# Kernel tuning notes

Hardware: AMD Instinct MI355X
Metric: run time of the kernel (lower is better)

The kernel has to match this reference:

```python
import jax, jax.numpy as jnp
import numpy as np
import math

NEG = -10000.0  # original uses -10000.0, not -inf

def setup_inputs() -> dict:
    key = jax.random.key(0)
    B, S, H, D = 2, 2048, 16, 128
    qkv = jax.random.normal(key, (B, S, 3, H, D), dtype=jnp.float32)
    return {"qkv": qkv}

def reference(qkv):
    # qkv: (B, S, 3, H, D); causal softmax attention, dropout p=0 (identity)
    B, S, _, H, D = qkv.shape
    q = qkv[:, :, 0]  # (B,S,H,D)
    k = qkv[:, :, 1]
    v = qkv[:, :, 2]
    softmax_scale = 1.0 / math.sqrt(D)
    # scores: (B, H, T, S)
    scores = jnp.einsum('bthd,bshd->bhts', q, k * softmax_scale)
    causal_mask = jnp.triu(jnp.full((S, S), NEG, dtype=scores.dtype), 1)
    scores = scores + causal_mask  # broadcast over (B,H)
    attention = jax.nn.softmax(scores, axis=-1)
    out = jnp.einsum('bhts,bshd->bthd', attention, v)  # (B,T,H,D)
    return out
```

## Files before the change

kernel.cpp:

```cpp
#include <hip/hip_runtime.h>
#include <hip/hip_bf16.h>
#include <math.h>

typedef __bf16 bf16;
typedef bf16 bf16x8 __attribute__((ext_vector_type(8)));
typedef float floatx4 __attribute__((ext_vector_type(4)));

#define MFMA16(a, b, c) __builtin_amdgcn_mfma_f32_16x16x32_bf16(a, b, c, 0, 0, 0)

constexpr int Bb = 2, Ss = 2048, Hh = 16, Dd = 128;
constexpr float SCALE = 0.08838834764831845f;

__global__ __launch_bounds__(256) void prep_pack(const float* __restrict__ qkv,
                                                 bf16* __restrict__ QP,
                                                 bf16* __restrict__ KP,
                                                 bf16* __restrict__ VP) {
  const int tid = threadIdx.x;
  const int w = tid >> 6, lane = tid & 63, quad = lane >> 4, l15 = lane & 15;
  const int qt = blockIdx.x, bh = blockIdx.y;
  const int b = bh >> 4, h = bh & 15;
  const int q0 = qt * 64;
  const size_t rs = (size_t)3 * Hh * Dd;
  const float* base = qkv + (size_t)b * Ss * rs + (size_t)h * Dd;

  {
    bf16* blob = QP + (size_t)(bh * 32 + qt) * 8192;
    const float* src = base + (size_t)(q0 + 4 * l15 + w) * rs;
    for (int kk = 0; kk < 4; ++kk) {
      const float* s8 = src + kk * 32 + quad * 8;
      float4 x0 = *(const float4*)s8, x1 = *(const float4*)(s8 + 4);
      bf16x8 f;
      f[0] = (bf16)(x0.x * SCALE); f[1] = (bf16)(x0.y * SCALE);
      f[2] = (bf16)(x0.z * SCALE); f[3] = (bf16)(x0.w * SCALE);
      f[4] = (bf16)(x1.x * SCALE); f[5] = (bf16)(x1.y * SCALE);
      f[6] = (bf16)(x1.z * SCALE); f[7] = (bf16)(x1.w * SCALE);
      *(bf16x8*)(blob + (size_t)(((w * 4 + kk) * 4 + quad) * 16 + l15) * 8) = f;
    }
  }

  const int ktg = qt * 2 + (w >> 1);
  {
    const int c = w & 1;
    bf16* blob = KP + (size_t)(bh * 64 + ktg) * 4096;
    const float* src = base + (size_t)(ktg * 32 + c * 16 + l15) * rs + Hh * Dd;
    for (int kk = 0; kk < 4; ++kk) {
      const float* s8 = src + kk * 32 + quad * 8;
      float4 x0 = *(const float4*)s8, x1 = *(const float4*)(s8 + 4);
      bf16x8 f;
      f[0] = (bf16)x0.x; f[1] = (bf16)x0.y; f[2] = (bf16)x0.z; f[3] = (bf16)x0.w;
      f[4] = (bf16)x1.x; f[5] = (bf16)x1.y; f[6] = (bf16)x1.z; f[7] = (bf16)x1.w;
      *(bf16x8*)(blob + (size_t)(((c * 4 + kk) * 4 + quad) * 16 + l15) * 8) = f;
    }
  }
  {
    bf16* blob = VP + (size_t)(bh * 64 + ktg) * 4096;
    const float* src = base + 2 * Hh * Dd;
    for (int ti = 0; ti < 4; ++ti) {
      const int t = (w & 1) * 4 + ti;
      const int d = t * 16 + l15;
      bf16x8 f;
      for (int j = 0; j < 8; ++j)
        f[j] = (bf16)src[(size_t)(ktg * 32 + quad * 8 + j) * rs + d];
      *(bf16x8*)(blob + (size_t)((t * 4 + quad) * 16 + l15) * 8) = f;
    }
  }
}

__device__ __forceinline__ void cp1k(const bf16* src, bf16* dst, int lane) {
  __builtin_amdgcn_global_load_lds(
      (__attribute__((address_space(1))) void*)(src + lane * 8),
      (__attribute__((address_space(3))) void*)dst, 16, 0, 0);
}

__global__ __launch_bounds__(256) void attn_fwd(const bf16* __restrict__ QP,
                                                const bf16* __restrict__ KP,
                                                const bf16* __restrict__ VP,
                                                float* __restrict__ out) {
  __shared__ bf16 Kl[2][4096];
  __shared__ bf16 Vl[2][4096];
  __shared__ bf16 Pl[4 * 16 * 40];

  const int tid = threadIdx.x;
  const int w = tid >> 6, lane = tid & 63, quad = lane >> 4, l15 = lane & 15;
  const int qt = (gridDim.x - 1) - blockIdx.x;
  const int bh = blockIdx.y;
  const int b = bh >> 4, h = bh & 15;
  const int q0 = qt * 64;

  bf16x8 qf[4];
  {
    const bf16* qp = QP + (size_t)(bh * 32 + qt) * 8192;
    for (int kk = 0; kk < 4; ++kk)
      qf[kk] = *(const bf16x8*)(qp + (size_t)(((w * 4 + kk) * 4 + quad) * 16 + l15) * 8);
  }

  floatx4 acc_o[8];
  for (int t = 0; t < 8; ++t) acc_o[t] = (floatx4){0.f, 0.f, 0.f, 0.f};
  float l_part[4] = {0.f, 0.f, 0.f, 0.f};

  const int ntiles = 2 * qt + 2;
  const size_t bh64 = (size_t)bh * 64;
  bf16* pw = &Pl[w * 640];

  auto stage = [&](int kt, int nb) {
    const bf16* kblob = KP + (bh64 + kt) * 4096;
    const bf16* vblob = VP + (bh64 + kt) * 4096;
    if (w < 2) {
      for (int i = 0; i < 4; ++i) {
        const int g = w * 4 + i;
        cp1k(kblob + g * 512, &Kl[nb][g * 512], lane);
      }
    } else {
      for (int i = 0; i < 4; ++i) {
        const int g = (w - 2) * 4 + i;
        cp1k(vblob + g * 512, &Vl[nb][g * 512], lane);
      }
    }
  };

  stage(0, 0);
  __syncthreads();

  for (int kt = 0; kt < ntiles; ++kt) {
    const int nb = kt & 1;
    if (kt + 1 < ntiles) stage(kt + 1, nb ^ 1);

    floatx4 sacc[2];
    sacc[0] = (floatx4){0.f, 0.f, 0.f, 0.f};
    sacc[1] = (floatx4){0.f, 0.f, 0.f, 0.f};
    for (int c = 0; c < 2; ++c)
      for (int kk = 0; kk < 4; ++kk) {
        bf16x8 bfrag = *(const bf16x8*)(&Kl[nb][((c * 4 + kk) * 64 + lane) * 8]);
        sacc[c] = MFMA16(qf[kk], bfrag, sacc[c]);
      }

    float p[2][4];
    const int kbase = kt * 32;
    if (kt >= 2 * qt) {
      for (int c = 0; c < 2; ++c) {
        const int colg = kbase + c * 16 + l15;
        for (int r = 0; r < 4; ++r) {
          const int rowg = q0 + 4 * (quad * 4 + r) + w;
          const float s = (colg > rowg) ? -10000.f : sacc[c][r];
          p[c][r] = __expf(s);
        }
      }
    } else {
      for (int c = 0; c < 2; ++c)
        for (int r = 0; r < 4; ++r) p[c][r] = __expf(sacc[c][r]);
    }
    for (int r = 0; r < 4; ++r) l_part[r] += p[0][r] + p[1][r];

    for (int c = 0; c < 2; ++c)
      for (int r = 0; r < 4; ++r)
        pw[(quad * 4 + r) * 40 + c * 16 + l15] = (bf16)p[c][r];

    bf16x8 af = *(const bf16x8*)(&Pl[w * 640 + l15 * 40 + quad * 8]);
    for (int t = 0; t < 8; ++t) {
      bf16x8 bfrag = *(const bf16x8*)(&Vl[nb][(t * 64 + lane) * 8]);
      acc_o[t] = MFMA16(af, bfrag, acc_o[t]);
    }

    __syncthreads();
  }

  float rl[4];
  for (int r = 0; r < 4; ++r) {
    float l = l_part[r];
    for (int off = 1; off < 16; off <<= 1) l += __shfl_xor(l, off);
    rl[r] = 1.0f / l;
  }
  for (int r = 0; r < 4; ++r) {
    const int rowg = q0 + 4 * (quad * 4 + r) + w;
    float* op = out + ((size_t)(b * Ss + rowg) * Hh + h) * Dd + l15;
    for (int t = 0; t < 8; ++t) op[t * 16] = acc_o[t][r] * rl[r];
  }
}

extern "C" void kernel_launch(void* const* d_in, const int* in_sizes, int n_in,
                              void* d_out, int out_size, void* d_ws, size_t ws_size,
                              hipStream_t stream) {
  const float* qkv = (const float*)d_in[0];
  float* out = (float*)d_out;
  bf16* QP = (bf16*)d_ws;
  bf16* KP = QP + (size_t)8 * 1024 * 1024;
  bf16* VP = KP + (size_t)8 * 1024 * 1024;

  dim3 grid(32, 32);
  prep_pack<<<grid, 256, 0, stream>>>(qkv, QP, KP, VP);
  attn_fwd<<<grid, 256, 0, stream>>>(QP, KP, VP, out);
}
```

Before: 251.6 us.

## Process two query tiles per block and transpose V through LDS in prep

The attention kernel now handles 128 query rows per block as two 64-row sub-tiles. Each staged K/V tile is reused for both, halving the global-to-LDS K/V traffic, and the upper sub-tile is skipped on diagonal-only tiles. The prep kernel first loads V rows with coalesced float4 reads into an LDS buffer and then builds the transposed blob from LDS, replacing strided scalar global reads. The cost is double the accumulator registers (a launch bound of 3 is requested), a grid of half as many blocks, and coarser causal load imbalance.

Result: no change. 250.5 us (-0.5%).

```diff
diff --git a/kernel.cpp b/kernel.cpp
--- a/kernel.cpp
+++ b/kernel.cpp
@@ -15,6 +15,8 @@
                                                  bf16* __restrict__ QP,
                                                  bf16* __restrict__ KP,
                                                  bf16* __restrict__ VP) {
+  __shared__ bf16 Vt[64 * 136];
+
   const int tid = threadIdx.x;
   const int w = tid >> 6, lane = tid & 63, quad = lane >> 4, l15 = lane & 15;
   const int qt = blockIdx.x, bh = blockIdx.y;
@@ -22,6 +24,15 @@
   const int q0 = qt * 64;
   const size_t rs = (size_t)3 * Hh * Dd;
   const float* base = qkv + (size_t)b * Ss * rs + (size_t)h * Dd;
+
+  for (int idx = tid; idx < 64 * 32; idx += 256) {
+    const int row = idx >> 5;
+    const int c4 = (idx & 31) << 2;
+    const float* p = base + (size_t)(q0 + row) * rs + 2 * Hh * Dd + c4;
+    float4 x = *(const float4*)p;
+    bf16* d = Vt + row * 136 + c4;
+    d[0] = (bf16)x.x; d[1] = (bf16)x.y; d[2] = (bf16)x.z; d[3] = (bf16)x.w;
+  }
 
   {
     bf16* blob = QP + (size_t)(bh * 32 + qt) * 8192;
@@ -52,15 +63,17 @@
       *(bf16x8*)(blob + (size_t)(((c * 4 + kk) * 4 + quad) * 16 + l15) * 8) = f;
     }
   }
+
+  __syncthreads();
+
   {
     bf16* blob = VP + (size_t)(bh * 64 + ktg) * 4096;
-    const float* src = base + 2 * Hh * Dd;
+    const int kloc = (w >> 1) * 32;
     for (int ti = 0; ti < 4; ++ti) {
       const int t = (w & 1) * 4 + ti;
       const int d = t * 16 + l15;
       bf16x8 f;
-      for (int j = 0; j < 8; ++j)
-        f[j] = (bf16)src[(size_t)(ktg * 32 + quad * 8 + j) * rs + d];
+      for (int j = 0; j < 8; ++j) f[j] = Vt[(kloc + quad * 8 + j) * 136 + d];
       *(bf16x8*)(blob + (size_t)((t * 4 + quad) * 16 + l15) * 8) = f;
     }
   }
@@ -72,35 +85,36 @@
       (__attribute__((address_space(3))) void*)dst, 16, 0, 0);
 }
 
-__global__ __launch_bounds__(256) void attn_fwd(const bf16* __restrict__ QP,
-                                                const bf16* __restrict__ KP,
-                                                const bf16* __restrict__ VP,
-                                                float* __restrict__ out) {
+__global__ __launch_bounds__(256, 3) void attn_fwd(const bf16* __restrict__ QP,
+                                                   const bf16* __restrict__ KP,
+                                                   const bf16* __restrict__ VP,
+                                                   float* __restrict__ out) {
   __shared__ bf16 Kl[2][4096];
   __shared__ bf16 Vl[2][4096];
-  __shared__ bf16 Pl[4 * 16 * 40];
+  __shared__ bf16 Pl[4 * 32 * 40];
 
   const int tid = threadIdx.x;
   const int w = tid >> 6, lane = tid & 63, quad = lane >> 4, l15 = lane & 15;
   const int qt = (gridDim.x - 1) - blockIdx.x;
   const int bh = blockIdx.y;
   const int b = bh >> 4, h = bh & 15;
-  const int q0 = qt * 64;
-
-  bf16x8 qf[4];
-  {
-    const bf16* qp = QP + (size_t)(bh * 32 + qt) * 8192;
+  const int q0 = qt * 128;
+
+  bf16x8 qf[2][4];
+  for (int u = 0; u < 2; ++u) {
+    const bf16* qp = QP + (size_t)(bh * 32 + 2 * qt + u) * 8192;
     for (int kk = 0; kk < 4; ++kk)
-      qf[kk] = *(const bf16x8*)(qp + (size_t)(((w * 4 + kk) * 4 + quad) * 16 + l15) * 8);
-  }
-
-  floatx4 acc_o[8];
-  for (int t = 0; t < 8; ++t) acc_o[t] = (floatx4){0.f, 0.f, 0.f, 0.f};
-  float l_part[4] = {0.f, 0.f, 0.f, 0.f};
-
-  const int ntiles = 2 * qt + 2;
+      qf[u][kk] = *(const bf16x8*)(qp + (size_t)(((w * 4 + kk) * 4 + quad) * 16 + l15) * 8);
+  }
+
+  floatx4 acc_o[2][8];
+  for (int u = 0; u < 2; ++u)
+    for (int t = 0; t < 8; ++t) acc_o[u][t] = (floatx4){0.f, 0.f, 0.f, 0.f};
+  float l_part[2][4] = {{0.f, 0.f, 0.f, 0.f}, {0.f, 0.f, 0.f, 0.f}};
+
+  const int ntiles = 4 * qt + 4;
   const size_t bh64 = (size_t)bh * 64;
-  bf16* pw = &Pl[w * 640];
+  bf16* pw = &Pl[w * 1280];
 
   auto stage = [&](int kt, int nb) {
     const bf16* kblob = KP + (bh64 + kt) * 4096;
@@ -125,55 +139,83 @@
     const int nb = kt & 1;
     if (kt + 1 < ntiles) stage(kt + 1, nb ^ 1);
 
-    floatx4 sacc[2];
-    sacc[0] = (floatx4){0.f, 0.f, 0.f, 0.f};
-    sacc[1] = (floatx4){0.f, 0.f, 0.f, 0.f};
+    const bool do0 = (kt <= 4 * qt + 1);
+    const bool mask0 = (kt >= 4 * qt);
+    const bool mask1 = (kt >= 4 * qt + 2);
+    const int kbase = kt * 32;
+
+    floatx4 s0[2], s1[2];
+    s0[0] = s0[1] = s1[0] = s1[1] = (floatx4){0.f, 0.f, 0.f, 0.f};
     for (int c = 0; c < 2; ++c)
       for (int kk = 0; kk < 4; ++kk) {
         bf16x8 bfrag = *(const bf16x8*)(&Kl[nb][((c * 4 + kk) * 64 + lane) * 8]);
-        sacc[c] = MFMA16(qf[kk], bfrag, sacc[c]);
-      }
-
-    float p[2][4];
-    const int kbase = kt * 32;
-    if (kt >= 2 * qt) {
-      for (int c = 0; c < 2; ++c) {
-        const int colg = kbase + c * 16 + l15;
-        for (int r = 0; r < 4; ++r) {
-          const int rowg = q0 + 4 * (quad * 4 + r) + w;
-          const float s = (colg > rowg) ? -10000.f : sacc[c][r];
-          p[c][r] = __expf(s);
+        if (do0) s0[c] = MFMA16(qf[0][kk], bfrag, s0[c]);
+        s1[c] = MFMA16(qf[1][kk], bfrag, s1[c]);
+      }
+
+    if (do0) {
+      float p[2][4];
+      if (mask0) {
+        for (int c = 0; c < 2; ++c) {
+          const int colg = kbase + c * 16 + l15;
+          for (int r = 0; r < 4; ++r) {
+            const int rowg = q0 + 4 * (quad * 4 + r) + w;
+            p[c][r] = __expf((colg > rowg) ? -10000.f : s0[c][r]);
+          }
         }
-      }
-    } else {
+      } else {
+        for (int c = 0; c < 2; ++c)
+          for (int r = 0; r < 4; ++r) p[c][r] = __expf(s0[c][r]);
+      }
+      for (int r = 0; r < 4; ++r) l_part[0][r] += p[0][r] + p[1][r];
       for (int c = 0; c < 2; ++c)
-        for (int r = 0; r < 4; ++r) p[c][r] = __expf(sacc[c][r]);
-    }
-    for (int r = 0; r < 4; ++r) l_part[r] += p[0][r] + p[1][r];
-
-    for (int c = 0; c < 2; ++c)
-      for (int r = 0; r < 4; ++r)
-        pw[(quad * 4 + r) * 40 + c * 16 + l15] = (bf16)p[c][r];
-
-    bf16x8 af = *(const bf16x8*)(&Pl[w * 640 + l15 * 40 + quad * 8]);
+        for (int r = 0; r < 4; ++r)
+          pw[(quad * 4 + r) * 40 + c * 16 + l15] = (bf16)p[c][r];
+    }
+    {
+      float p[2][4];
+      if (mask1) {
+        for (int c = 0; c < 2; ++c) {
+          const int colg = kbase + c * 16 + l15;
+          for (int r = 0; r < 4; ++r) {
+            const int rowg = q0 + 64 + 4 * (quad * 4 + r) + w;
+            p[c][r] = __expf((colg > rowg) ? -10000.f : s1[c][r]);
+          }
+        }
+      } else {
+        for (int c = 0; c < 2; ++c)
+          for (int r = 0; r < 4; ++r) p[c][r] = __expf(s1[c][r]);
+      }
+      for (int r = 0; r < 4; ++r) l_part[1][r] += p[0][r] + p[1][r];
+      for (int c = 0; c < 2; ++c)
+        for (int r = 0; r < 4; ++r)
+          pw[(16 + quad * 4 + r) * 40 + c * 16 + l15] = (bf16)p[c][r];
+    }
+
+    bf16x8 af0, af1;
+    if (do0) af0 = *(const bf16x8*)(&Pl[w * 1280 + l15 * 40 + quad * 8]);
+    af1 = *(const bf16x8*)(&Pl[w * 1280 + (16 + l15) * 40 + quad * 8]);
     for (int t = 0; t < 8; ++t) {
-      bf16x8 bfrag = *(const bf16x8*)(&Vl[nb][(t * 64 + lane) * 8]);
-      acc_o[t] = MFMA16(af, bfrag, acc_o[t]);
+      bf16x8 vfrag = *(const bf16x8*)(&Vl[nb][(t * 64 + lane) * 8]);
+      if (do0) acc_o[0][t] = MFMA16(af0, vfrag, acc_o[0][t]);
+      acc_o[1][t] = MFMA16(af1, vfrag, acc_o[1][t]);
     }
 
     __syncthreads();
   }
 
-  float rl[4];
-  for (int r = 0; r < 4; ++r) {
-    float l = l_part[r];
-    for (int off = 1; off < 16; off <<= 1) l += __shfl_xor(l, off);
-    rl[r] = 1.0f / l;
-  }
-  for (int r = 0; r < 4; ++r) {
-    const int rowg = q0 + 4 * (quad * 4 + r) + w;
-    float* op = out + ((size_t)(b * Ss + rowg) * Hh + h) * Dd + l15;
-    for (int t = 0; t < 8; ++t) op[t * 16] = acc_o[t][r] * rl[r];
+  for (int u = 0; u < 2; ++u) {
+    float rl[4];
+    for (int r = 0; r < 4; ++r) {
+      float l = l_part[u][r];
+      for (int off = 1; off < 16; off <<= 1) l += __shfl_xor(l, off);
+      rl[r] = 1.0f / l;
+    }
+    for (int r = 0; r < 4; ++r) {
+      const int rowg = q0 + u * 64 + 4 * (quad * 4 + r) + w;
+      float* op = out + ((size_t)(b * Ss + rowg) * Hh + h) * Dd + l15;
+      for (int t = 0; t < 8; ++t) op[t * 16] = acc_o[u][t][r] * rl[r];
+    }
   }
 }
 
@@ -186,7 +228,6 @@
   bf16* KP = QP + (size_t)8 * 1024 * 1024;
   bf16* VP = KP + (size_t)8 * 1024 * 1024;
 
-  dim3 grid(32, 32);
-  prep_pack<<<grid, 256, 0, stream>>>(qkv, QP, KP, VP);
-  attn_fwd<<<grid, 256, 0, stream>>>(QP, KP, VP, out);
-}
+  prep_pack<<<dim3(32, 32), 256, 0, stream>>>(qkv, QP, KP, VP);
+  attn_fwd<<<dim3(16, 32), 256, 0, stream>>>(QP, KP, VP, out);
+}
```
